# Kernel optimization log

Measured on AMD Instinct MI355X. Metric: run time of the kernel, lower is better.

The kernel has to match this reference:

```python
import jax, jax.numpy as jnp
import numpy as np

N_NODES = 131072
N_EDGES = 262144
N_GRAPHS = 4096
EMB = 300
N_LAYER = 5
N_TASKS = 1
NUM_ATOM_TYPE = 120
NUM_CHIRALITY = 3
NUM_BOND_TYPE = 6   # includes self-loop type 4
NUM_BOND_DIR = 3
SELF_LOOP_TYPE = 4
BN_EPS = 1e-5


def setup_inputs() -> dict:
    key = jax.random.key(0)
    ks = jax.random.split(key, 20)
    x = jnp.stack([
        jax.random.randint(ks[0], (N_NODES,), 0, NUM_ATOM_TYPE, dtype=jnp.int32),
        jax.random.randint(ks[1], (N_NODES,), 0, NUM_CHIRALITY, dtype=jnp.int32),
    ], axis=1)
    edge_index = jax.random.randint(ks[2], (2, N_EDGES), 0, N_NODES, dtype=jnp.int32)
    edge_attr = jnp.stack([
        jax.random.randint(ks[3], (N_EDGES,), 0, 4, dtype=jnp.int32),
        jax.random.randint(ks[4], (N_EDGES,), 0, NUM_BOND_DIR, dtype=jnp.int32),
    ], axis=1)
    # sorted batch vector, every graph non-empty (32 nodes per graph)
    batch = jnp.repeat(jnp.arange(N_GRAPHS, dtype=jnp.int32), N_NODES // N_GRAPHS)
    s = 0.05
    params = {
        'atom_emb0': jax.random.normal(ks[5], (NUM_ATOM_TYPE, EMB), jnp.float32) * s,
        'atom_emb1': jax.random.normal(ks[6], (NUM_CHIRALITY, EMB), jnp.float32) * s,
        'bond_emb0': jax.random.normal(ks[7], (N_LAYER, NUM_BOND_TYPE, EMB), jnp.float32) * s,
        'bond_emb1': jax.random.normal(ks[8], (N_LAYER, NUM_BOND_DIR, EMB), jnp.float32) * s,
        'W1': jax.random.normal(ks[9], (N_LAYER, EMB, 2 * EMB), jnp.float32) * s,
        'b1': jnp.zeros((N_LAYER, 2 * EMB), jnp.float32),
        'W2': jax.random.normal(ks[10], (N_LAYER, 2 * EMB, EMB), jnp.float32) * s,
        'b2': jnp.zeros((N_LAYER, EMB), jnp.float32),
        'bn_gamma': jnp.ones((N_LAYER, EMB), jnp.float32),
        'bn_beta': jnp.zeros((N_LAYER, EMB), jnp.float32),
        'head_W1': jax.random.normal(ks[11], (EMB, EMB // 2), jnp.float32) * s,
        'head_b1': jnp.zeros((EMB // 2,), jnp.float32),
        'head_W2': jax.random.normal(ks[12], (EMB // 2, N_TASKS), jnp.float32) * s,
        'head_b2': jnp.zeros((N_TASKS,), jnp.float32),
    }
    return dict(x=x, edge_index=edge_index, edge_attr=edge_attr, batch=batch,
                num_graphs=N_GRAPHS, **params)


def _gnn_forward(x, edge_index, edge_attr, batch, num_graphs,
                 atom_emb0, atom_emb1, bond_emb0, bond_emb1,
                 W1, b1, W2, b2, bn_gamma, bn_beta,
                 head_W1, head_b1, head_W2, head_b2):
    n = x.shape[0]
    L = W1.shape[0]
    # add self loops with bond type SELF_LOOP_TYPE
    loop = jnp.arange(n, dtype=edge_index.dtype)
    src = jnp.concatenate([edge_index[0], loop])
    dst = jnp.concatenate([edge_index[1], loop])
    ea0 = jnp.concatenate([edge_attr[:, 0], jnp.full((n,), SELF_LOOP_TYPE, edge_attr.dtype)])
    ea1 = jnp.concatenate([edge_attr[:, 1], jnp.zeros((n,), edge_attr.dtype)])

    h = atom_emb0[x[:, 0]] + atom_emb1[x[:, 1]]  # [N, EMB]
    for l in range(L):
        e = bond_emb0[l][ea0] + bond_emb1[l][ea1]           # [E+N, EMB]
        msg = h[src] + e                                     # gather + add
        agg = jax.ops.segment_sum(msg, dst, num_segments=n)  # [N, EMB]
        hid = jax.nn.relu(agg @ W1[l] + b1[l])
        h2 = hid @ W2[l] + b2[l]
        # BatchNorm1d (training-mode batch stats)
        mean = jnp.mean(h2, axis=0)
        var = jnp.var(h2, axis=0)
        h2 = (h2 - mean) * jax.lax.rsqrt(var + BN_EPS) * bn_gamma[l] + bn_beta[l]
        h = h2 if l == L - 1 else jax.nn.relu(h2)
    # super_node_rep: last node of each graph (batch is sorted)
    last_idx = jax.ops.segment_max(jnp.arange(n), batch, num_segments=num_graphs)
    sup = h[last_idx]                                        # [G, EMB]
    out = jax.nn.elu(sup @ head_W1 + head_b1) @ head_W2 + head_b2
    return out                                               # [G, num_tasks]


def reference(x, edge_index, edge_attr, batch, num_graphs,
              atom_emb0, atom_emb1, bond_emb0, bond_emb1,
              W1, b1, W2, b2, bn_gamma, bn_beta,
              head_W1, head_b1, head_W2, head_b2):
    return _gnn_forward(x, edge_index, edge_attr, batch, num_graphs,
                        atom_emb0, atom_emb1, bond_emb0, bond_emb1,
                        W1, b1, W2, b2, bn_gamma, bn_beta,
                        head_W1, head_b1, head_W2, head_b2)
```

## Files before the change

kernel.cpp:

```cpp
#include <hip/hip_runtime.h>
#include <hip/hip_bf16.h>

#define NN 131072
#define NE 262144
#define NG 4096
#define EMB 300
#define HS 320
#define K1 320
#define N1 640
#define K2E 608
#define N2P 384
#define NLAYER 5
#define NRB (NN / 128)

typedef __attribute__((ext_vector_type(8))) short short8;
typedef __attribute__((ext_vector_type(4))) float f32x4;
typedef __attribute__((ext_vector_type(4))) unsigned short ushort4v;

__device__ __forceinline__ void gload_lds16(const void* g, void* l) {
  __builtin_amdgcn_global_load_lds((const __attribute__((address_space(1))) void*)g,
                                   (__attribute__((address_space(3))) void*)l, 16, 0, 0);
}
__device__ __forceinline__ float b2f(unsigned short u) {
  return __uint_as_float(((unsigned)u) << 16);
}
__device__ __forceinline__ unsigned short f2b(float x) {
  __hip_bfloat16 b = __float2bfloat16(x);
  return *(unsigned short*)&b;
}


__global__ void prep_w1(const float* __restrict__ W1, __hip_bfloat16* __restrict__ W1T) {
  int idx = blockIdx.x * 256 + threadIdx.x;
  if (idx >= NLAYER * N1 * K1) return;
  int l = idx / (N1 * K1); int r = idx % (N1 * K1);
  int n = r / K1; int k = r % K1;
  float v = (n < 600 && k < 300) ? W1[(size_t)(l * 300 + k) * 600 + n] : 0.f;
  W1T[idx] = __float2bfloat16(v);
}

__global__ void prep_w2(const float* __restrict__ W2, __hip_bfloat16* __restrict__ W2T) {
  int idx = blockIdx.x * 256 + threadIdx.x;
  if (idx >= NLAYER * N2P * N1) return;
  int l = idx / (N2P * N1); int r = idx % (N2P * N1);
  int n = r / N1; int k = r % N1;
  float v = (n < 300 && k < 600) ? W2[(size_t)(l * 600 + k) * 300 + n] : 0.f;
  W2T[idx] = __float2bfloat16(v);
}

__global__ void prep_bias(const float* __restrict__ b1, const float* __restrict__ b2,
                          float* __restrict__ b1p, float* __restrict__ b2p) {
  int idx = blockIdx.x * 256 + threadIdx.x;
  if (idx < NLAYER * N1) {
    int l = idx / N1, n = idx % N1;
    b1p[idx] = (n < 600) ? b1[l * 600 + n] : 0.f;
  } else {
    int k = idx - NLAYER * N1;
    if (k < NLAYER * N2P) {
      int l = k / N2P, n = k % N2P;
      b2p[k] = (n < 300) ? b2[l * 300 + n] : 0.f;
    }
  }
}

__global__ void prep_etab(const float* __restrict__ bond0, const float* __restrict__ bond1,
                          float* __restrict__ etabg) {
  int idx = blockIdx.x * 256 + threadIdx.x;
  if (idx >= NLAYER * 13 * HS) return;
  int l = idx / (13 * HS); int r = idx % (13 * HS);
  int c = r / HS; int ch = r % HS;
  float val = 0.f;
  if (ch < EMB) {
    int t0 = (c < 12) ? (c / 3) : 4;
    int t1 = (c < 12) ? (c % 3) : 0;
    val = bond0[(size_t)(l * 6 + t0) * EMB + ch] + bond1[(size_t)(l * 3 + t1) * EMB + ch];
  }
  etabg[idx] = val;
}

__global__ void init_h(const int* __restrict__ x, const float* __restrict__ ae0,
                       const float* __restrict__ ae1, __hip_bfloat16* __restrict__ h) {
  int v = blockIdx.x; int t = threadIdx.x;
  int x0 = x[2 * v], x1 = x[2 * v + 1];
  for (int c = t; c < HS; c += 256)
    h[(size_t)v * HS + c] = __float2bfloat16(c < EMB ? ae0[x0 * EMB + c] + ae1[x1 * EMB + c] : 0.f);
}


__global__ void count_edges(const int* __restrict__ ei, int* __restrict__ counts) {
  int j = blockIdx.x * 256 + threadIdx.x;
  if (j >= NE) return;
  atomicAdd(&counts[ei[NE + j]], 1);
}

__global__ void scan_block(const int* __restrict__ counts, int* __restrict__ indptr,
                           int* __restrict__ blockSums) {
  __shared__ int s[256];
  int b = blockIdx.x, t = threadIdx.x;
  int base = b * 1024 + t * 4;
  int4 c = *(const int4*)&counts[base];
  int tsum = c.x + c.y + c.z + c.w;
  s[t] = tsum;
  __syncthreads();
  for (int off = 1; off < 256; off <<= 1) {
    int v = (t >= off) ? s[t - off] : 0;
    __syncthreads();
    s[t] += v;
    __syncthreads();
  }
  int excl = (t == 0) ? 0 : s[t - 1];
  indptr[base + 0] = excl;
  indptr[base + 1] = excl + c.x;
  indptr[base + 2] = excl + c.x + c.y;
  indptr[base + 3] = excl + c.x + c.y + c.z;
  if (t == 255) blockSums[b] = s[255];
}

__global__ void scan_top(const int* __restrict__ blockSums, int* __restrict__ blockOff) {
  __shared__ int s[128];
  int t = threadIdx.x;
  s[t] = blockSums[t];
  __syncthreads();
  for (int off = 1; off < 128; off <<= 1) {
    int v = (t >= off) ? s[t - off] : 0;
    __syncthreads();
    s[t] += v;
    __syncthreads();
  }
  blockOff[t] = (t == 0) ? 0 : s[t - 1];
}

__global__ void scan_add(int* __restrict__ indptr, const int* __restrict__ blockOff) {
  int b = blockIdx.x, t = threadIdx.x;
  int off = blockOff[b];
  int base = b * 1024 + t * 4;
  indptr[base + 0] += off; indptr[base + 1] += off;
  indptr[base + 2] += off; indptr[base + 3] += off;
  if (b == 127 && t == 255) indptr[NN] = NE;
}

__global__ void scatter_edges(const int* __restrict__ ei, const int* __restrict__ ea,
                              int* __restrict__ cursor, int* __restrict__ epacked) {
  int j = blockIdx.x * 256 + threadIdx.x;
  if (j >= NE) return;
  int dst = ei[NE + j];
  int src = ei[j];
  int c = ea[2 * j] * 3 + ea[2 * j + 1];
  int pos = atomicAdd(&cursor[dst], 1);
  epacked[pos] = src | (c << 17);
}

__global__ void last_idx_kernel(const int* __restrict__ batch, int* __restrict__ lastidx) {
  int i = blockIdx.x * 256 + threadIdx.x;
  if (i >= NN) return;
  int b = batch[i];
  if (i == NN - 1 || batch[i + 1] != b) lastidx[b] = i;
}

template<int BN>
__global__ __launch_bounds__(1024)
void aggregate_kernel(const __hip_bfloat16* __restrict__ hg, const int* __restrict__ indptr,
                      const int* __restrict__ epacked, const float* __restrict__ etabg,
                      const float* __restrict__ bnsc, const float* __restrict__ bnsh,
                      __hip_bfloat16* __restrict__ agg) {
  __shared__ float etab[13 * HS];
  const int tid = threadIdx.x;
#pragma unroll
  for (int idx = tid; idx < 13 * HS; idx += 1024)
    etab[idx] = etabg[idx];
  __syncthreads();
  const int wid = tid >> 6, lane = tid & 63;
  const int cA = lane * 4, cB = 256 + lane;
  const unsigned short* h = (const unsigned short*)hg;

  f32x4 scA = {1.f, 1.f, 1.f, 1.f}, shA = {0.f, 0.f, 0.f, 0.f};
  float scB = 1.f, shB = 0.f;
  if (BN) {
    scA = *(const f32x4*)&bnsc[cA]; shA = *(const f32x4*)&bnsh[cA];
    scB = bnsc[cB]; shB = bnsh[cB];
  }
  auto trA = [&](float x, int k) -> float {
    if (BN) x = fmaxf(fmaf(x, scA[k], shA[k]), 0.f);
    return x;
  };
  auto trB = [&](float x) -> float {
    if (BN) x = fmaxf(fmaf(x, scB, shB), 0.f);
    return x;
  };
  const float* es = etab + 12 * HS;

  for (int it = 0; it < 4; ++it) {
    const int v = blockIdx.x * 64 + it * 16 + wid;
    const unsigned short* hv = h + (size_t)v * HS;
    ushort4v pA = *(const ushort4v*)(hv + cA);
    unsigned short pB = hv[cB];
    float a0 = trA(b2f(pA[0]), 0) + es[cA];
    float a1 = trA(b2f(pA[1]), 1) + es[cA + 1];
    float a2 = trA(b2f(pA[2]), 2) + es[cA + 2];
    float a3 = trA(b2f(pA[3]), 3) + es[cA + 3];
    float a4 = trB(b2f(pB)) + es[cB];

    const int jb = indptr[v], je = indptr[v + 1];
    int j = jb;
    for (; j + 2 <= je; j += 2) {
      int p0 = epacked[j], p1 = epacked[j + 1];
      const unsigned short* h0 = h + (size_t)(p0 & (NN - 1)) * HS;
      const unsigned short* h1 = h + (size_t)(p1 & (NN - 1)) * HS;
      ushort4v q0 = *(const ushort4v*)(h0 + cA);
      ushort4v q1 = *(const ushort4v*)(h1 + cA);
      unsigned short r0 = h0[cB], r1 = h1[cB];
      const float* e0 = etab + (p0 >> 17) * HS;
      const float* e1 = etab + (p1 >> 17) * HS;
      a0 += trA(b2f(q0[0]), 0) + e0[cA]     + trA(b2f(q1[0]), 0) + e1[cA];
      a1 += trA(b2f(q0[1]), 1) + e0[cA + 1] + trA(b2f(q1[1]), 1) + e1[cA + 1];
      a2 += trA(b2f(q0[2]), 2) + e0[cA + 2] + trA(b2f(q1[2]), 2) + e1[cA + 2];
      a3 += trA(b2f(q0[3]), 3) + e0[cA + 3] + trA(b2f(q1[3]), 3) + e1[cA + 3];
      a4 += trB(b2f(r0)) + e0[cB] + trB(b2f(r1)) + e1[cB];
    }
    if (j < je) {
      int p0 = epacked[j];
      const unsigned short* h0 = h + (size_t)(p0 & (NN - 1)) * HS;
      ushort4v q0 = *(const ushort4v*)(h0 + cA);
      unsigned short r0 = h0[cB];
      const float* e0 = etab + (p0 >> 17) * HS;
      a0 += trA(b2f(q0[0]), 0) + e0[cA];
      a1 += trA(b2f(q0[1]), 1) + e0[cA + 1];
      a2 += trA(b2f(q0[2]), 2) + e0[cA + 2];
      a3 += trA(b2f(q0[3]), 3) + e0[cA + 3];
      a4 += trB(b2f(r0)) + e0[cB];
    }

    unsigned short* av = (unsigned short*)agg + (size_t)v * HS;
    ushort4v o; o[0] = f2b(a0); o[1] = f2b(a1); o[2] = f2b(a2); o[3] = f2b(a3);
    *(ushort4v*)(av + cA) = o;
    av[cB] = f2b(a4);
  }
}

template<int RELU, int STATS, int NBN, int KSTRIDE, int KEXT, int BCOLS, int NWAVES>
__global__ __launch_bounds__(NWAVES * 64)
void gemm_kernel(const short* __restrict__ A, const short* __restrict__ BT,
                 const float* __restrict__ bias, __hip_bfloat16* __restrict__ Cout,
                 float* __restrict__ part, int outStride, int outBound, int rbBase) {
  constexpr int THREADS = NWAVES * 64;
  constexpr int BSH = BCOLS * 32;
  constexpr int BUFSZ = 4096 + BSH;
  constexpr int NCW = NWAVES / 2;
  constexpr int WCOL = BCOLS / NCW;
  constexpr int NF = WCOL / 16;
  __shared__ short smem[3 * BUFSZ];
  __shared__ float sred[STATS ? BCOLS : 1][2];
  const int tid = threadIdx.x;
  const int wid = tid >> 6, lane = tid & 63;
  const int wm = wid / NCW, wn = wid % NCW;
  f32x4 acc[4][NF] = {};

  const int cpx = gridDim.x >> 3;
  const int logical = (blockIdx.x & 7) * cpx + (blockIdx.x >> 3);
  const int bn = logical % NBN;
  const int bm = logical / NBN;

  const short* Ag = A + (size_t)bm * 128 * KSTRIDE;
  const short* Bg = BT + (size_t)bn * BCOLS * KSTRIDE;
  const int r2 = tid >> 2;
  const int ksw = ((tid & 3) ^ ((tid >> 3) & 3)) * 8;
  const int arow_h = lane & 15;
  const int koffR = (((lane >> 4) ^ ((arow_h >> 1) & 3)) * 8);

  const short* Ao = Ag + (size_t)r2 * KSTRIDE + ksw;
  const short* Bo = Bg + (size_t)r2 * KSTRIDE + ksw;

  auto stage = [&](int buf, int kt) {
    short* s = smem + buf * BUFSZ;
    gload_lds16(Ao + kt, s + tid * 8);
    if constexpr (THREADS == 256)
      gload_lds16(Ao + kt + 64 * KSTRIDE, s + 2048 + tid * 8);
    gload_lds16(Bo + kt, s + 4096 + tid * 8);
  };

  constexpr int NT = KEXT / 32;
  stage(0, 0);
  stage(1, 32);
#pragma unroll
  for (int t = 0; t < NT; ++t) {
    if (t + 1 < NT) {
      if constexpr (THREADS == 256) asm volatile("s_waitcnt vmcnt(3)" ::: "memory");
      else                          asm volatile("s_waitcnt vmcnt(2)" ::: "memory");
    } else {
      asm volatile("s_waitcnt vmcnt(0)" ::: "memory");
    }
    __builtin_amdgcn_sched_barrier(0);
    __builtin_amdgcn_s_barrier();
    const int rb = t % 3;
    if (t + 2 < NT) stage((t + 2) % 3, (t + 2) * 32);
    const short* sA = smem + rb * BUFSZ + wm * 2048;
    const short* sB = smem + rb * BUFSZ + 4096 + wn * (WCOL * 32);
    short8 af[4], bf[NF];
#pragma unroll
    for (int i = 0; i < 4; i++) af[i] = *(const short8*)&sA[(arow_h + i * 16) * 32 + koffR];
#pragma unroll
    for (int j = 0; j < NF; j++) bf[j] = *(const short8*)&sB[(arow_h + j * 16) * 32 + koffR];
#pragma unroll
    for (int i = 0; i < 4; i++)
#pragma unroll
      for (int j = 0; j < NF; j++)
        acc[i][j] = __builtin_amdgcn_mfma_f32_16x16x32_bf16(af[i], bf[j], acc[i][j], 0, 0, 0);
    __builtin_amdgcn_sched_barrier(0);
  }

  const int row0 = bm * 128 + wm * 64 + (lane >> 4) * 4;
  const int col0 = bn * BCOLS + wn * WCOL + (lane & 15);
  float bs[NF];
#pragma unroll
  for (int j = 0; j < NF; j++) bs[j] = bias[col0 + j * 16];
  float ssum[NF], ssq[NF];
#pragma unroll
  for (int j = 0; j < NF; j++) { ssum[j] = 0.f; ssq[j] = 0.f; }
  if (STATS) {
    if (tid < BCOLS) { sred[tid][0] = 0.f; sred[tid][1] = 0.f; }
    __syncthreads();
  }
#pragma unroll
  for (int i = 0; i < 4; i++) {
#pragma unroll
    for (int p = 0; p < 4; p++) {
      const size_t row = row0 + i * 16 + p;
#pragma unroll
      for (int j = 0; j < NF; j++) {
        const int col = col0 + j * 16;
        float v = acc[i][j][p] + bs[j];
        if (STATS) { ssum[j] += v; ssq[j] += v * v; }
        if (RELU) v = fmaxf(v, 0.f);
        if (col < outBound)
          Cout[row * (size_t)outStride + col] = __float2bfloat16(v);
      }
    }
  }
  if (STATS) {
#pragma unroll
    for (int j = 0; j < NF; j++) {
      const int cw = wn * WCOL + j * 16 + (lane & 15);
      atomicAdd(&sred[cw][0], ssum[j]);
      atomicAdd(&sred[cw][1], ssq[j]);
    }
    __syncthreads();
    if (tid < BCOLS) {
      const int col = bn * BCOLS + tid;
      if (col < EMB) {
        const int rb2 = rbBase + bm;
        part[(size_t)col * (2 * NRB) + rb2] = sred[tid][0];
        part[(size_t)col * (2 * NRB) + NRB + rb2] = sred[tid][1];
      }
    }
  }
}

__global__ __launch_bounds__(256)
void bn_finalize(const float* __restrict__ part, const float* __restrict__ gamma,
                 const float* __restrict__ beta, float* __restrict__ bnsc,
                 float* __restrict__ bnsh) {
  __shared__ float rs[256], rq[256];
  const int c = blockIdx.x, t = threadIdx.x;
  if (c >= EMB) {
    if (t == 0) { bnsc[c] = 0.f; bnsh[c] = 0.f; }
    return;
  }
  float s = 0.f, q = 0.f;
  for (int rb = t; rb < NRB; rb += 256) {
    s += part[(size_t)c * (2 * NRB) + rb];
    q += part[(size_t)c * (2 * NRB) + NRB + rb];
  }
  rs[t] = s; rq[t] = q;
  __syncthreads();
  for (int off = 128; off > 0; off >>= 1) {
    if (t < off) { rs[t] += rs[t + off]; rq[t] += rq[t + off]; }
    __syncthreads();
  }
  if (t == 0) {
    float mean = rs[0] / (float)NN;
    float var = rq[0] / (float)NN - mean * mean;
    float sc = rsqrtf(var + 1e-5f) * gamma[c];
    bnsc[c] = sc;
    bnsh[c] = beta[c] - mean * sc;
  }
}

__global__ __launch_bounds__(256)
void head_kernel(const __hip_bfloat16* __restrict__ h, const int* __restrict__ lastidx,
                 const float* __restrict__ bnsc4, const float* __restrict__ bnsh4,
                 const float* __restrict__ hW1, const float* __restrict__ hb1,
                 const float* __restrict__ hW2, const float* __restrict__ hb2,
                 float* __restrict__ out) {
  __shared__ float sup[EMB];
  __shared__ float red[256];
  int g = blockIdx.x, t = threadIdx.x;
  int v = lastidx[g];
  for (int c = t; c < EMB; c += 256)
    sup[c] = b2f(((const unsigned short*)h)[(size_t)v * HS + c]) * bnsc4[c] + bnsh4[c];
  __syncthreads();
  float val = 0.f;
  if (t < 150) {
    float acc = hb1[t];
    for (int k = 0; k < EMB; k++) acc += sup[k] * hW1[k * 150 + t];
    float e = (acc > 0.f) ? acc : (expf(acc) - 1.f);
    val = e * hW2[t];
  }
  red[t] = val;
  __syncthreads();
  for (int off = 128; off > 0; off >>= 1) {
    if (t < off) red[t] += red[t + off];
    __syncthreads();
  }
  if (t == 0) out[g] = red[0] + hb2[0];
}


extern "C" void kernel_launch(void* const* d_in, const int* in_sizes, int n_in,
                              void* d_out, int out_size, void* d_ws, size_t ws_size,
                              hipStream_t stream) {
  const int* x      = (const int*)d_in[0];
  const int* ei     = (const int*)d_in[1];
  const int* ea     = (const int*)d_in[2];
  const int* batch  = (const int*)d_in[3];
  const float* atom0 = (const float*)d_in[5];
  const float* atom1 = (const float*)d_in[6];
  const float* bond0 = (const float*)d_in[7];
  const float* bond1 = (const float*)d_in[8];
  const float* W1    = (const float*)d_in[9];
  const float* b1    = (const float*)d_in[10];
  const float* W2    = (const float*)d_in[11];
  const float* b2    = (const float*)d_in[12];
  const float* gamma = (const float*)d_in[13];
  const float* beta  = (const float*)d_in[14];
  const float* hW1   = (const float*)d_in[15];
  const float* hb1   = (const float*)d_in[16];
  const float* hW2   = (const float*)d_in[17];
  const float* hb2   = (const float*)d_in[18];
  float* out = (float*)d_out;

  char* p = (char*)d_ws;
  auto carve = [&](size_t b) -> void* {
    void* r = (void*)p;
    p += (b + 255) & ~(size_t)255;
    return r;
  };
  __hip_bfloat16* agg = (__hip_bfloat16*)carve((size_t)NN * HS * 2);
  __hip_bfloat16* h   = (__hip_bfloat16*)carve((size_t)NN * HS * 2);
  __hip_bfloat16* W1T = (__hip_bfloat16*)carve((size_t)NLAYER * N1 * K1 * 2);
  __hip_bfloat16* W2T = (__hip_bfloat16*)carve((size_t)NLAYER * N2P * N1 * 2);
  float* b1p          = (float*)carve((size_t)NLAYER * N1 * 4);
  float* b2p          = (float*)carve((size_t)NLAYER * N2P * 4);
  float* etabg        = (float*)carve((size_t)NLAYER * 13 * HS * 4);
  float* part         = (float*)carve((size_t)EMB * 2 * NRB * 4);
  float* bnsc         = (float*)carve((size_t)NLAYER * HS * 4);
  float* bnsh         = (float*)carve((size_t)NLAYER * HS * 4);
  int* counts         = (int*)carve((size_t)NN * 4);
  int* indptr         = (int*)carve((size_t)(NN + 1) * 4);
  int* cursor         = (int*)carve((size_t)NN * 4);
  int* epacked        = (int*)carve((size_t)NE * 4);
  int* blockSums      = (int*)carve(128 * 4);
  int* blockOff       = (int*)carve(128 * 4);
  int* lastidx        = (int*)carve((size_t)NG * 4);

  size_t used = (size_t)(p - (char*)d_ws);
  size_t avail = (ws_size > used + 4096) ? (ws_size - used - 4096) : 0;
  int CHUNK = 16384;
  if (avail >= (size_t)65536 * N1 * 2) CHUNK = 65536;
  else if (avail >= (size_t)32768 * N1 * 2) CHUNK = 32768;
  __hip_bfloat16* hid = (__hip_bfloat16*)carve((size_t)CHUNK * N1 * 2);

  hipMemsetAsync(counts, 0, (size_t)NN * 4, stream);

  prep_w1<<<(NLAYER * N1 * K1 + 255) / 256, 256, 0, stream>>>(W1, W1T);
  prep_w2<<<(NLAYER * N2P * N1 + 255) / 256, 256, 0, stream>>>(W2, W2T);
  prep_bias<<<(NLAYER * (N1 + N2P) + 255) / 256, 256, 0, stream>>>(b1, b2, b1p, b2p);
  prep_etab<<<(NLAYER * 13 * HS + 255) / 256, 256, 0, stream>>>(bond0, bond1, etabg);
  init_h<<<NN, 256, 0, stream>>>(x, atom0, atom1, h);

  count_edges<<<NE / 256, 256, 0, stream>>>(ei, counts);
  scan_block<<<128, 256, 0, stream>>>(counts, indptr, blockSums);
  scan_top<<<1, 128, 0, stream>>>(blockSums, blockOff);
  scan_add<<<128, 256, 0, stream>>>(indptr, blockOff);
  hipMemcpyAsync(cursor, indptr, (size_t)NN * 4, hipMemcpyDeviceToDevice, stream);
  scatter_edges<<<NE / 256, 256, 0, stream>>>(ei, ea, cursor, epacked);
  last_idx_kernel<<<NN / 256, 256, 0, stream>>>(batch, lastidx);

  for (int l = 0; l < NLAYER; l++) {
    if (l == 0)
      aggregate_kernel<0><<<NN / 64, 1024, 0, stream>>>(
          h, indptr, epacked, etabg + (size_t)l * 13 * HS, nullptr, nullptr, agg);
    else
      aggregate_kernel<1><<<NN / 64, 1024, 0, stream>>>(
          h, indptr, epacked, etabg + (size_t)l * 13 * HS,
          bnsc + (size_t)(l - 1) * HS, bnsh + (size_t)(l - 1) * HS, agg);
    for (int c0 = 0; c0 < NN; c0 += CHUNK) {
      gemm_kernel<1, 0, 5, K1, K1, 128, 8><<<(CHUNK / 128) * 5, 512, 0, stream>>>(
          (const short*)(agg + (size_t)c0 * HS),
          (const short*)(W1T + (size_t)l * N1 * K1), b1p + l * N1,
          hid, nullptr, N1, N1, 0);
      gemm_kernel<0, 1, 5, N1, K2E, 64, 4><<<(CHUNK / 128) * 5, 256, 0, stream>>>(
          (const short*)hid,
          (const short*)(W2T + (size_t)l * N2P * N1), b2p + l * N2P,
          h + (size_t)c0 * HS, part, HS, HS, c0 / 128);
    }
    bn_finalize<<<HS, 256, 0, stream>>>(part, gamma + (size_t)l * EMB, beta + (size_t)l * EMB,
                                        bnsc + (size_t)l * HS, bnsh + (size_t)l * HS);
  }

  head_kernel<<<NG, 256, 0, stream>>>(h, lastidx, bnsc + 4 * HS, bnsh + 4 * HS,
                                      hW1, hb1, hW2, hb2, out);
}
```

Measured before the change: 1.493 ms.

## Unify GEMM tiles to 128x64 with 8 waves, each wave computing 64x16

Both MLP GEMMs now use a single 128x64 output tile with 512 threads. Each wave computes a 64x16 sub-tile, so the first GEMM launches twice as many blocks with narrower N tiles. The second GEMM moves from 4 to 8 waves. The aim is more parallelism and occupancy and simpler staging. The cost is less B-fragment reuse per A load (one MFMA column per wave) and twice the A-tile reloads across N tiles for the first GEMM, which lowers arithmetic intensity.

```diff
diff --git a/kernel.cpp b/kernel.cpp
--- a/kernel.cpp
+++ b/kernel.cpp
@@ -237,23 +237,18 @@
   }
 }
 
-template<int RELU, int STATS, int NBN, int KSTRIDE, int KEXT, int BCOLS, int NWAVES>
-__global__ __launch_bounds__(NWAVES * 64)
+template<int RELU, int STATS, int NBN, int KSTRIDE, int KEXT>
+__global__ __launch_bounds__(512)
 void gemm_kernel(const short* __restrict__ A, const short* __restrict__ BT,
                  const float* __restrict__ bias, __hip_bfloat16* __restrict__ Cout,
                  float* __restrict__ part, int outStride, int outBound, int rbBase) {
-  constexpr int THREADS = NWAVES * 64;
-  constexpr int BSH = BCOLS * 32;
-  constexpr int BUFSZ = 4096 + BSH;
-  constexpr int NCW = NWAVES / 2;
-  constexpr int WCOL = BCOLS / NCW;
-  constexpr int NF = WCOL / 16;
+  constexpr int BUFSZ = 4096 + 2048;
   __shared__ short smem[3 * BUFSZ];
-  __shared__ float sred[STATS ? BCOLS : 1][2];
+  __shared__ float sred[STATS ? 64 : 1][2];
   const int tid = threadIdx.x;
   const int wid = tid >> 6, lane = tid & 63;
-  const int wm = wid / NCW, wn = wid % NCW;
-  f32x4 acc[4][NF] = {};
+  const int wm = wid >> 2, wn = wid & 3;
+  f32x4 acc[4] = {};
 
   const int cpx = gridDim.x >> 3;
   const int logical = (blockIdx.x & 7) * cpx + (blockIdx.x >> 3);
@@ -261,7 +256,7 @@
   const int bm = logical / NBN;
 
   const short* Ag = A + (size_t)bm * 128 * KSTRIDE;
-  const short* Bg = BT + (size_t)bn * BCOLS * KSTRIDE;
+  const short* Bg = BT + (size_t)bn * 64 * KSTRIDE;
   const int r2 = tid >> 2;
   const int ksw = ((tid & 3) ^ ((tid >> 3) & 3)) * 8;
   const int arow_h = lane & 15;
@@ -273,9 +268,8 @@
   auto stage = [&](int buf, int kt) {
     short* s = smem + buf * BUFSZ;
     gload_lds16(Ao + kt, s + tid * 8);
-    if constexpr (THREADS == 256)
-      gload_lds16(Ao + kt + 64 * KSTRIDE, s + 2048 + tid * 8);
-    gload_lds16(Bo + kt, s + 4096 + tid * 8);
+    if (tid < 256)
+      gload_lds16(Bo + kt, s + 4096 + tid * 8);
   };
 
   constexpr int NT = KEXT / 32;
@@ -284,8 +278,8 @@
 #pragma unroll
   for (int t = 0; t < NT; ++t) {
     if (t + 1 < NT) {
-      if constexpr (THREADS == 256) asm volatile("s_waitcnt vmcnt(3)" ::: "memory");
-      else                          asm volatile("s_waitcnt vmcnt(2)" ::: "memory");
+      if (wid < 4) asm volatile("s_waitcnt vmcnt(2)" ::: "memory");
+      else         asm volatile("s_waitcnt vmcnt(1)" ::: "memory");
     } else {
       asm volatile("s_waitcnt vmcnt(0)" ::: "memory");
     }
@@ -294,30 +288,23 @@
     const int rb = t % 3;
     if (t + 2 < NT) stage((t + 2) % 3, (t + 2) * 32);
     const short* sA = smem + rb * BUFSZ + wm * 2048;
-    const short* sB = smem + rb * BUFSZ + 4096 + wn * (WCOL * 32);
-    short8 af[4], bf[NF];
+    const short* sB = smem + rb * BUFSZ + 4096 + wn * (16 * 32);
+    short8 af[4], bf;
 #pragma unroll
     for (int i = 0; i < 4; i++) af[i] = *(const short8*)&sA[(arow_h + i * 16) * 32 + koffR];
-#pragma unroll
-    for (int j = 0; j < NF; j++) bf[j] = *(const short8*)&sB[(arow_h + j * 16) * 32 + koffR];
+    bf = *(const short8*)&sB[arow_h * 32 + koffR];
 #pragma unroll
     for (int i = 0; i < 4; i++)
-#pragma unroll
-      for (int j = 0; j < NF; j++)
-        acc[i][j] = __builtin_amdgcn_mfma_f32_16x16x32_bf16(af[i], bf[j], acc[i][j], 0, 0, 0);
+      acc[i] = __builtin_amdgcn_mfma_f32_16x16x32_bf16(af[i], bf, acc[i], 0, 0, 0);
     __builtin_amdgcn_sched_barrier(0);
   }
 
   const int row0 = bm * 128 + wm * 64 + (lane >> 4) * 4;
-  const int col0 = bn * BCOLS + wn * WCOL + (lane & 15);
-  float bs[NF];
-#pragma unroll
-  for (int j = 0; j < NF; j++) bs[j] = bias[col0 + j * 16];
-  float ssum[NF], ssq[NF];
-#pragma unroll
-  for (int j = 0; j < NF; j++) { ssum[j] = 0.f; ssq[j] = 0.f; }
+  const int col0 = bn * 64 + wn * 16 + (lane & 15);
+  const float bs = bias[col0];
+  float ssum = 0.f, ssq = 0.f;
   if (STATS) {
-    if (tid < BCOLS) { sred[tid][0] = 0.f; sred[tid][1] = 0.f; }
+    if (tid < 64) { sred[tid][0] = 0.f; sred[tid][1] = 0.f; }
     __syncthreads();
   }
 #pragma unroll
@@ -325,27 +312,20 @@
 #pragma unroll
     for (int p = 0; p < 4; p++) {
       const size_t row = row0 + i * 16 + p;
-#pragma unroll
-      for (int j = 0; j < NF; j++) {
-        const int col = col0 + j * 16;
-        float v = acc[i][j][p] + bs[j];
-        if (STATS) { ssum[j] += v; ssq[j] += v * v; }
-        if (RELU) v = fmaxf(v, 0.f);
-        if (col < outBound)
-          Cout[row * (size_t)outStride + col] = __float2bfloat16(v);
-      }
+      float v = acc[i][p] + bs;
+      if (STATS) { ssum += v; ssq += v * v; }
+      if (RELU) v = fmaxf(v, 0.f);
+      if (col0 < outBound)
+        Cout[row * (size_t)outStride + col0] = __float2bfloat16(v);
     }
   }
   if (STATS) {
-#pragma unroll
-    for (int j = 0; j < NF; j++) {
-      const int cw = wn * WCOL + j * 16 + (lane & 15);
-      atomicAdd(&sred[cw][0], ssum[j]);
-      atomicAdd(&sred[cw][1], ssq[j]);
-    }
-    __syncthreads();
-    if (tid < BCOLS) {
-      const int col = bn * BCOLS + tid;
+    const int cw = wn * 16 + (lane & 15);
+    atomicAdd(&sred[cw][0], ssum);
+    atomicAdd(&sred[cw][1], ssq);
+    __syncthreads();
+    if (tid < 64) {
+      const int col = bn * 64 + tid;
       if (col < EMB) {
         const int rb2 = rbBase + bm;
         part[(size_t)col * (2 * NRB) + rb2] = sred[tid][0];
@@ -494,11 +474,11 @@
           h, indptr, epacked, etabg + (size_t)l * 13 * HS,
           bnsc + (size_t)(l - 1) * HS, bnsh + (size_t)(l - 1) * HS, agg);
     for (int c0 = 0; c0 < NN; c0 += CHUNK) {
-      gemm_kernel<1, 0, 5, K1, K1, 128, 8><<<(CHUNK / 128) * 5, 512, 0, stream>>>(
+      gemm_kernel<1, 0, 10, K1, K1><<<(CHUNK / 128) * 10, 512, 0, stream>>>(
           (const short*)(agg + (size_t)c0 * HS),
           (const short*)(W1T + (size_t)l * N1 * K1), b1p + l * N1,
           hid, nullptr, N1, N1, 0);
-      gemm_kernel<0, 1, 5, N1, K2E, 64, 4><<<(CHUNK / 128) * 5, 256, 0, stream>>>(
+      gemm_kernel<0, 1, 5, N1, K2E><<<(CHUNK / 128) * 5, 512, 0, stream>>>(
           (const short*)hid,
           (const short*)(W2T + (size_t)l * N2P * N1), b2p + l * N2P,
           h + (size_t)c0 * HS, part, HS, HS, c0 / 128);
```

Result: no change. 1.512 ms (+1.3%).
